# Kernel optimization log

Hardware: AMD Instinct MI355X
Metric: run time of the kernel (lower is better)

The kernel has to match this reference:

```python
import jax, jax.numpy as jnp
import numpy as np

N_EMBD = 768
N_HEAD = 12
EPS = 1e-5


def _layernorm(x, g, b):
    mu = x.mean(-1, keepdims=True)
    var = ((x - mu) ** 2).mean(-1, keepdims=True)
    return (x - mu) * jax.lax.rsqrt(var + EPS) * g + b


def setup_inputs() -> dict:
    key = jax.random.key(0)
    ks = jax.random.split(key, 8)
    C = N_EMBD
    s = lambda n: 0.02
    return {
        "x": jax.random.normal(ks[0], (8, 1024, C), jnp.float32),
        "ln1_g": jnp.ones((C,), jnp.float32),
        "ln1_b": jnp.zeros((C,), jnp.float32),
        "w_attn": jax.random.normal(ks[1], (C, 3 * C), jnp.float32) * 0.02,
        "b_attn": jnp.zeros((3 * C,), jnp.float32),
        "w_proj": jax.random.normal(ks[2], (C, C), jnp.float32) * 0.02,
        "b_proj": jnp.zeros((C,), jnp.float32),
        "ln2_g": jnp.ones((C,), jnp.float32),
        "ln2_b": jnp.zeros((C,), jnp.float32),
        "w_fc": jax.random.normal(ks[3], (C, 4 * C), jnp.float32) * 0.02,
        "b_fc": jnp.zeros((4 * C,), jnp.float32),
        "w_fc2": jax.random.normal(ks[4], (4 * C, C), jnp.float32) * 0.02,
        "b_fc2": jnp.zeros((C,), jnp.float32),
    }


def reference(x, ln1_g, ln1_b, w_attn, b_attn, w_proj, b_proj,
              ln2_g, ln2_b, w_fc, b_fc, w_fc2, b_fc2):
    B, T, C = x.shape
    H = N_HEAD
    hd = C // H

    # --- attention branch (NOTE: source has NO 1/sqrt(d) scaling) ---
    h = _layernorm(x, ln1_g, ln1_b)
    qkv = h @ w_attn + b_attn                      # [B,T,3C]
    q, k, v = jnp.split(qkv, 3, axis=-1)
    q = q.reshape(B, T, H, hd)
    k = k.reshape(B, T, H, hd)
    v = v.reshape(B, T, H, hd)
    wei = jnp.einsum('bthd,bshd->bhts', q, k)      # [B,H,T,T], unscaled
    causal = jnp.tril(jnp.ones((T, T), bool))
    wei = jnp.where(causal, wei, -jnp.inf)
    wei = jax.nn.softmax(wei, axis=-1)
    out = jnp.einsum('bhts,bshd->bthd', wei, v)    # [B,T,H,hd]
    out = out.reshape(B, T, C)
    attn_out = out @ w_proj + b_proj
    x = x + attn_out

    # --- MLP branch ---
    h = _layernorm(x, ln2_g, ln2_b)
    h = jax.nn.gelu(h @ w_fc + b_fc, approximate=True)
    x = x + (h @ w_fc2 + b_fc2)
    return x
```

## Files before the change

### kernel.cpp

```cpp
#include <hip/hip_runtime.h>
#include <math.h>

#define N_EMBD 768
#define T_SEQ  1024
#define BATCH  8
#define NHEAD  12
#define HD     64
#define EPS    1e-5f
#define M_TOK  (BATCH * T_SEQ)

typedef unsigned short u16;
typedef __attribute__((ext_vector_type(8))) short          s16x8;
typedef __attribute__((ext_vector_type(8))) unsigned short u16x8;
typedef __attribute__((ext_vector_type(4))) float          f32x4;

#define GLDS(gp, lp) \
    __builtin_amdgcn_global_load_lds( \
        (const __attribute__((address_space(1))) void*)(gp), \
        (__attribute__((address_space(3))) void*)(lp), 16, 0, 0)

__device__ __forceinline__ u16 f2bf(float f) {
    unsigned int u = __float_as_uint(f);
    u += 0x7fffu + ((u >> 16) & 1u);
    return (u16)(u >> 16);
}

__global__ __launch_bounds__(256) void wconv(const float* __restrict__ in,
                                             u16* __restrict__ out, int R, int C) {
    __shared__ float tile[64][65];
    int t = threadIdx.x;
    int r0 = blockIdx.y * 64, c0 = blockIdx.x * 64;
    int rl = t >> 4, c4 = (t & 15) * 4;
#pragma unroll
    for (int i = 0; i < 4; i++) {
        float4 v = *(const float4*)(in + (size_t)(r0 + rl + i * 16) * C + c0 + c4);
        tile[rl + i * 16][c4 + 0] = v.x;
        tile[rl + i * 16][c4 + 1] = v.y;
        tile[rl + i * 16][c4 + 2] = v.z;
        tile[rl + i * 16][c4 + 3] = v.w;
    }
    __syncthreads();
#pragma unroll
    for (int i = 0; i < 4; i++) {
        int crow = rl + i * 16;
        ushort4 s4;
        s4.x = f2bf(tile[c4 + 0][crow]);
        s4.y = f2bf(tile[c4 + 1][crow]);
        s4.z = f2bf(tile[c4 + 2][crow]);
        s4.w = f2bf(tile[c4 + 3][crow]);
        *(ushort4*)(out + (size_t)(c0 + crow) * R + r0 + c4) = s4;
    }
}

__global__ __launch_bounds__(256) void ln_bf16(const float* __restrict__ x,
                                               const float* __restrict__ g,
                                               const float* __restrict__ b,
                                               u16* __restrict__ out) {
    int row = blockIdx.x;
    int tid = threadIdx.x;
    const float* xr = x + (size_t)row * N_EMBD;
    float v0 = xr[tid], v1 = xr[tid + 256], v2 = xr[tid + 512];
    float s1 = v0 + v1 + v2;
    float s2 = v0 * v0 + v1 * v1 + v2 * v2;
    __shared__ float red1[4], red2[4];
#pragma unroll
    for (int o = 32; o > 0; o >>= 1) {
        s1 += __shfl_down(s1, o);
        s2 += __shfl_down(s2, o);
    }
    if ((tid & 63) == 0) { red1[tid >> 6] = s1; red2[tid >> 6] = s2; }
    __syncthreads();
    float mean = (red1[0] + red1[1] + red1[2] + red1[3]) * (1.0f / N_EMBD);
    float ms   = (red2[0] + red2[1] + red2[2] + red2[3]) * (1.0f / N_EMBD);
    float rs = rsqrtf(ms - mean * mean + EPS);
    u16* orow = out + (size_t)row * N_EMBD;
    orow[tid]       = f2bf((v0 - mean) * rs * g[tid]       + b[tid]);
    orow[tid + 256] = f2bf((v1 - mean) * rs * g[tid + 256] + b[tid + 256]);
    orow[tid + 512] = f2bf((v2 - mean) * rs * g[tid + 512] + b[tid + 512]);
}

template <int MODE>
__global__ __launch_bounds__(256) void gemm_bf16(const u16* __restrict__ A,
                                                 const u16* __restrict__ Bt,
                                                 const float* __restrict__ bias,
                                                 const float* __restrict__ res,
                                                 void* __restrict__ outp,
                                                 int M, int N, int K) {
    __shared__ u16 As[128][64];
    __shared__ u16 Bs[128][64];
    int tid = threadIdx.x;
    int l = tid & 63, w = tid >> 6;
    int lr = l & 15, lg = l >> 4;
    int bm = blockIdx.y * 128, bn = blockIdx.x * 128;
    int wr = (w >> 1) * 64, wc = (w & 1) * 64;
    int srow = l >> 3;
    int scol = (l & 7) * 8;
    f32x4 acc[4][4] = {};
    for (int k0 = 0; k0 < K; k0 += 64) {
        __syncthreads();
#pragma unroll
        for (int i = 0; i < 4; i++) {
            int c = i * 4 + w;
            int row = c * 8 + srow;
            GLDS(A  + (size_t)(bm + row) * K + k0 + scol, &As[c * 8][0]);
            GLDS(Bt + (size_t)(bn + row) * K + k0 + scol, &Bs[c * 8][0]);
        }
        __syncthreads();
#pragma unroll
        for (int kk = 0; kk < 2; kk++) {
            s16x8 af[4], bf[4];
#pragma unroll
            for (int i = 0; i < 4; i++) {
                af[i] = *(const s16x8*)&As[wr + i * 16 + lr][kk * 32 + lg * 8];
                bf[i] = *(const s16x8*)&Bs[wc + i * 16 + lr][kk * 32 + lg * 8];
            }
#pragma unroll
            for (int mi = 0; mi < 4; mi++)
#pragma unroll
                for (int nj = 0; nj < 4; nj++)
                    acc[mi][nj] = __builtin_amdgcn_mfma_f32_16x16x32_bf16(
                        af[mi], bf[nj], acc[mi][nj], 0, 0, 0);
        }
    }
#pragma unroll
    for (int mi = 0; mi < 4; mi++)
#pragma unroll
        for (int nj = 0; nj < 4; nj++)
#pragma unroll
            for (int r = 0; r < 4; r++) {
                int row = bm + wr + mi * 16 + lg * 4 + r;
                int col = bn + wc + nj * 16 + lr;
                float v = acc[mi][nj][r] + bias[col];
                if (MODE == 1) {
                    float u = v + 0.044715f * v * v * v;
                    v = 0.5f * v * (1.0f + tanhf(0.7978845608028654f * u));
                }
                if (MODE == 2) {
                    v += res[(size_t)row * N + col];
                    ((float*)outp)[(size_t)row * N + col] = v;
                } else {
                    ((u16*)outp)[(size_t)row * N + col] = f2bf(v);
                }
            }
}

#define QBLK 128
#define SBLK 64
__global__ __launch_bounds__(256) void attn_mfma(const u16* __restrict__ qkv,
                                                 u16* __restrict__ outp) {
    __shared__ u16 Kl[SBLK][64];
    __shared__ u16 Vt[HD][72];
    __shared__ u16 Pl[4][32][72];
    int tid = threadIdx.x;
    int w = tid >> 6, l = tid & 63;
    int lr = l & 15, lg = l >> 4;
    int h = blockIdx.y, b = blockIdx.z;
    size_t bbase = (size_t)b * T_SEQ * (3 * N_EMBD);

    for (int half = 0; half < 2; half++) {
        int qt = half == 0 ? blockIdx.x : 7 - blockIdx.x;
        int q0 = qt * QBLK;

        s16x8 qf[2][2];
#pragma unroll
        for (int rg = 0; rg < 2; rg++)
#pragma unroll
            for (int kk = 0; kk < 2; kk++) {
                int row = q0 + w * 32 + rg * 16 + lr;
                qf[rg][kk] = *(const s16x8*)(qkv + bbase + (size_t)row * (3 * N_EMBD) +
                                             h * HD + kk * 32 + lg * 8);
            }
        f32x4 oacc[2][4] = {};
        float mrun[2][4], lrun[2][4];
#pragma unroll
        for (int rg = 0; rg < 2; rg++)
#pragma unroll
            for (int r = 0; r < 4; r++) { mrun[rg][r] = -1e30f; lrun[rg][r] = 0.f; }

        int nt = 2 * qt + 2;
        for (int st = 0; st < nt; st++) {
            int s0 = st * SBLK;
#pragma unroll
            for (int i = 0; i < 2; i++) {
                int c = i * 4 + w;
                int row = c * 8 + (l >> 3);
                GLDS(qkv + bbase + (size_t)(s0 + row) * (3 * N_EMBD) + N_EMBD + h * HD + (l & 7) * 8,
                     &Kl[c * 8][0]);
            }
#pragma unroll
            for (int i = 0; i < 2; i++) {
                int c = i * 256 + tid;
                int sr = c >> 3, d0 = (c & 7) * 8;
                u16x8 vv = *(const u16x8*)(qkv + bbase + (size_t)(s0 + sr) * (3 * N_EMBD) +
                                           2 * N_EMBD + h * HD + d0);
                int sz = ((sr >> 3) ^ (d0 >> 3)) * 8 + (sr & 7);
#pragma unroll
                for (int j = 0; j < 8; j++) Vt[d0 + j][sz] = vv[j];
            }
            __syncthreads();
            f32x4 sacc[2][4] = {};
#pragma unroll
            for (int kk = 0; kk < 2; kk++) {
                s16x8 kf[4];
#pragma unroll
                for (int nj = 0; nj < 4; nj++)
                    kf[nj] = *(const s16x8*)&Kl[nj * 16 + lr][kk * 32 + lg * 8];
#pragma unroll
                for (int rg = 0; rg < 2; rg++)
#pragma unroll
                    for (int nj = 0; nj < 4; nj++)
                        sacc[rg][nj] = __builtin_amdgcn_mfma_f32_16x16x32_bf16(
                            qf[rg][kk], kf[nj], sacc[rg][nj], 0, 0, 0);
            }
#pragma unroll
            for (int rg = 0; rg < 2; rg++) {
                int qrow0 = q0 + w * 32 + rg * 16 + lg * 4;
                float mx[4];
#pragma unroll
                for (int r = 0; r < 4; r++) {
                    int qi = qrow0 + r;
                    float mv = -1e30f;
#pragma unroll
                    for (int nj = 0; nj < 4; nj++) {
                        int si = s0 + nj * 16 + lr;
                        float v = sacc[rg][nj][r];
                        v = (si <= qi) ? v : -1e30f;
                        sacc[rg][nj][r] = v;
                        mv = fmaxf(mv, v);
                    }
                    mx[r] = mv;
                }
#pragma unroll
                for (int d = 1; d < 16; d <<= 1)
#pragma unroll
                    for (int r = 0; r < 4; r++) mx[r] = fmaxf(mx[r], __shfl_xor(mx[r], d, 64));
                float rs[4];
#pragma unroll
                for (int r = 0; r < 4; r++) {
                    float mnew = fmaxf(mrun[rg][r], mx[r]);
                    float sc = __expf(mrun[rg][r] - mnew);
                    mrun[rg][r] = mnew;
                    float sum = 0.f;
#pragma unroll
                    for (int nj = 0; nj < 4; nj++) {
                        float p = __expf(sacc[rg][nj][r] - mnew);
                        sacc[rg][nj][r] = p;
                        sum += p;
                    }
                    rs[r] = sum;
                    lrun[rg][r] *= sc;
#pragma unroll
                    for (int nj = 0; nj < 4; nj++) oacc[rg][nj][r] *= sc;
                }
#pragma unroll
                for (int d = 1; d < 16; d <<= 1)
#pragma unroll
                    for (int r = 0; r < 4; r++) rs[r] += __shfl_xor(rs[r], d, 64);
#pragma unroll
                for (int r = 0; r < 4; r++) lrun[rg][r] += rs[r];
#pragma unroll
                for (int nj = 0; nj < 4; nj++)
#pragma unroll
                    for (int r = 0; r < 4; r++)
                        Pl[w][rg * 16 + lg * 4 + r][nj * 16 + lr] = f2bf(sacc[rg][nj][r]);
            }
            __syncthreads();
#pragma unroll
            for (int kk = 0; kk < 2; kk++) {
                s16x8 af[2], vf[4];
#pragma unroll
                for (int rg = 0; rg < 2; rg++)
                    af[rg] = *(const s16x8*)&Pl[w][rg * 16 + lr][kk * 32 + lg * 8];
#pragma unroll
                for (int nj = 0; nj < 4; nj++) {
                    int d = nj * 16 + lr;
                    int gs = (kk * 4 + lg) ^ (d >> 3);
                    vf[nj] = *(const s16x8*)&Vt[d][gs * 8];
                }
#pragma unroll
                for (int rg = 0; rg < 2; rg++)
#pragma unroll
                    for (int nj = 0; nj < 4; nj++)
                        oacc[rg][nj] = __builtin_amdgcn_mfma_f32_16x16x32_bf16(
                            af[rg], vf[nj], oacc[rg][nj], 0, 0, 0);
            }
            __syncthreads();
        }
#pragma unroll
        for (int rg = 0; rg < 2; rg++)
#pragma unroll
            for (int nj = 0; nj < 4; nj++)
#pragma unroll
                for (int r = 0; r < 4; r++) {
                    int row = q0 + w * 32 + rg * 16 + lg * 4 + r;
                    float v = oacc[rg][nj][r] / lrun[rg][r];
                    outp[(size_t)(b * T_SEQ + row) * N_EMBD + h * HD + nj * 16 + lr] = f2bf(v);
                }
    }
}

extern "C" void kernel_launch(void* const* d_in, const int* in_sizes, int n_in,
                              void* d_out, int out_size, void* d_ws, size_t ws_size,
                              hipStream_t stream) {
    (void)in_sizes; (void)n_in; (void)out_size; (void)ws_size;
    const float* x      = (const float*)d_in[0];
    const float* ln1_g  = (const float*)d_in[1];
    const float* ln1_b  = (const float*)d_in[2];
    const float* w_attn = (const float*)d_in[3];
    const float* b_attn = (const float*)d_in[4];
    const float* w_proj = (const float*)d_in[5];
    const float* b_proj = (const float*)d_in[6];
    const float* ln2_g  = (const float*)d_in[7];
    const float* ln2_b  = (const float*)d_in[8];
    const float* w_fc   = (const float*)d_in[9];
    const float* b_fc   = (const float*)d_in[10];
    const float* w_fc2  = (const float*)d_in[11];
    const float* b_fc2  = (const float*)d_in[12];
    float* out = (float*)d_out;
    u16* ws = (u16*)d_ws;

    u16* wTa  = ws;
    u16* wTp  = wTa + (size_t)2304 * 768;
    u16* wTf  = wTp + (size_t)768 * 768;
    u16* wTf2 = wTf + (size_t)3072 * 768;
    u16* hbuf = wTf2 + (size_t)768 * 3072;
    u16* abuf = hbuf + (size_t)M_TOK * N_EMBD;
    u16* big  = abuf + (size_t)M_TOK * N_EMBD;

    wconv<<<dim3(2304 / 64, 768 / 64), 256, 0, stream>>>(w_attn, wTa, 768, 2304);
    wconv<<<dim3(768 / 64, 768 / 64), 256, 0, stream>>>(w_proj, wTp, 768, 768);
    wconv<<<dim3(3072 / 64, 768 / 64), 256, 0, stream>>>(w_fc, wTf, 768, 3072);
    wconv<<<dim3(768 / 64, 3072 / 64), 256, 0, stream>>>(w_fc2, wTf2, 3072, 768);
    ln_bf16<<<M_TOK, 256, 0, stream>>>(x, ln1_g, ln1_b, hbuf);
    gemm_bf16<0><<<dim3(18, 64), 256, 0, stream>>>(hbuf, wTa, b_attn, nullptr, big,
                                                   M_TOK, 3 * N_EMBD, N_EMBD);
    attn_mfma<<<dim3(T_SEQ / QBLK / 2, NHEAD, BATCH), 256, 0, stream>>>(big, abuf);
    gemm_bf16<2><<<dim3(6, 64), 256, 0, stream>>>(abuf, wTp, b_proj, x, out,
                                                  M_TOK, N_EMBD, N_EMBD);
    ln_bf16<<<M_TOK, 256, 0, stream>>>(out, ln2_g, ln2_b, hbuf);
    gemm_bf16<1><<<dim3(24, 64), 256, 0, stream>>>(hbuf, wTf, b_fc, nullptr, big,
                                                   M_TOK, 4 * N_EMBD, N_EMBD);
    gemm_bf16<2><<<dim3(6, 64), 256, 0, stream>>>(big, wTf2, b_fc2, out, out,
                                                  M_TOK, N_EMBD, 4 * N_EMBD);
}
```

Before: 456.5 us.

## Double-buffer GEMM LDS tiles, swizzle block order, and use exp-based GELU

The bf16 GEMM now keeps two LDS buffers per operand. It issues the asynchronous global-to-LDS loads for the next K tile before running the MFMAs on the current one, so memory latency overlaps compute, and one barrier per iteration is removed. Workgroup IDs are remapped in groups of 8 to change which output tiles run together, aiming for better L2 reuse across the chiplets. The tanh GELU is rewritten in the equivalent form v - v/(1+exp(2a)) using __expf, which is cheaper. LDS usage doubles, which can lower occupancy.

After: 439.7 us. -3.7%, faster.

```diff
diff --git a/kernel.cpp b/kernel.cpp
--- a/kernel.cpp
+++ b/kernel.cpp
@@ -86,33 +86,46 @@
                                                  const float* __restrict__ res,
                                                  void* __restrict__ outp,
                                                  int M, int N, int K) {
-    __shared__ u16 As[128][64];
-    __shared__ u16 Bs[128][64];
+    __shared__ u16 As[2][128][64];
+    __shared__ u16 Bs[2][128][64];
     int tid = threadIdx.x;
     int l = tid & 63, w = tid >> 6;
     int lr = l & 15, lg = l >> 4;
-    int bm = blockIdx.y * 128, bn = blockIdx.x * 128;
+    int gx = gridDim.x, nwg = gx * gridDim.y;
+    int bid = blockIdx.y * gx + blockIdx.x;
+    int swz = (bid & 7) * (nwg >> 3) + (bid >> 3);
+    int bm = (swz / gx) * 128, bn = (swz % gx) * 128;
     int wr = (w >> 1) * 64, wc = (w & 1) * 64;
-    int srow = l >> 3;
-    int scol = (l & 7) * 8;
+    int srow = l >> 3, scol = (l & 7) * 8;
     f32x4 acc[4][4] = {};
-    for (int k0 = 0; k0 < K; k0 += 64) {
+    int nt = K / 64;
+#pragma unroll
+    for (int i = 0; i < 4; i++) {
+        int c = i * 4 + w;
+        int row = c * 8 + srow;
+        GLDS(A  + (size_t)(bm + row) * K + scol, &As[0][c * 8][0]);
+        GLDS(Bt + (size_t)(bn + row) * K + scol, &Bs[0][c * 8][0]);
+    }
+    int cur = 0;
+    for (int t = 0; t < nt; t++) {
         __syncthreads();
-#pragma unroll
-        for (int i = 0; i < 4; i++) {
-            int c = i * 4 + w;
-            int row = c * 8 + srow;
-            GLDS(A  + (size_t)(bm + row) * K + k0 + scol, &As[c * 8][0]);
-            GLDS(Bt + (size_t)(bn + row) * K + k0 + scol, &Bs[c * 8][0]);
+        if (t + 1 < nt) {
+            int k0 = (t + 1) * 64;
+#pragma unroll
+            for (int i = 0; i < 4; i++) {
+                int c = i * 4 + w;
+                int row = c * 8 + srow;
+                GLDS(A  + (size_t)(bm + row) * K + k0 + scol, &As[cur ^ 1][c * 8][0]);
+                GLDS(Bt + (size_t)(bn + row) * K + k0 + scol, &Bs[cur ^ 1][c * 8][0]);
+            }
         }
-        __syncthreads();
 #pragma unroll
         for (int kk = 0; kk < 2; kk++) {
             s16x8 af[4], bf[4];
 #pragma unroll
             for (int i = 0; i < 4; i++) {
-                af[i] = *(const s16x8*)&As[wr + i * 16 + lr][kk * 32 + lg * 8];
-                bf[i] = *(const s16x8*)&Bs[wc + i * 16 + lr][kk * 32 + lg * 8];
+                af[i] = *(const s16x8*)&As[cur][wr + i * 16 + lr][kk * 32 + lg * 8];
+                bf[i] = *(const s16x8*)&Bs[cur][wc + i * 16 + lr][kk * 32 + lg * 8];
             }
 #pragma unroll
             for (int mi = 0; mi < 4; mi++)
@@ -121,6 +134,7 @@
                     acc[mi][nj] = __builtin_amdgcn_mfma_f32_16x16x32_bf16(
                         af[mi], bf[nj], acc[mi][nj], 0, 0, 0);
         }
+        cur ^= 1;
     }
 #pragma unroll
     for (int mi = 0; mi < 4; mi++)
@@ -132,8 +146,8 @@
                 int col = bn + wc + nj * 16 + lr;
                 float v = acc[mi][nj][r] + bias[col];
                 if (MODE == 1) {
-                    float u = v + 0.044715f * v * v * v;
-                    v = 0.5f * v * (1.0f + tanhf(0.7978845608028654f * u));
+                    float u = 1.5957691216057308f * (v + 0.044715f * v * v * v);
+                    v = v - v / (1.0f + __expf(u));
                 }
                 if (MODE == 2) {
                     v += res[(size_t)row * N + col];
@@ -160,7 +174,6 @@
     for (int half = 0; half < 2; half++) {
         int qt = half == 0 ? blockIdx.x : 7 - blockIdx.x;
         int q0 = qt * QBLK;
-
         s16x8 qf[2][2];
 #pragma unroll
         for (int rg = 0; rg < 2; rg++)
```

## Double-buffer GEMM LDS tiles, XOR-swizzle LDS layout, cheaper GELU via exp

Applied to the files above, without the earlier changes.

The GEMM now keeps two LDS buffers and issues the global-to-LDS loads for tile t+2 while computing tile t, using vmcnt waits and raw barriers in place of the two __syncthreads per k-step. The global source column is XOR-swizzled by row so the MFMA fragment reads from LDS avoid bank conflicts, and the attention K tile gets the same swizzle. The tanh-based GELU is rewritten algebraically as v - v/(1+exp(2u)) using __expf. Together these aim to hide memory latency and cut LDS conflicts, at the cost of twice the GEMM LDS footprint (lower occupancy) and slightly different GELU rounding.

Result: faster. 395.4 us (-13.4%).

```diff
diff --git a/kernel.cpp b/kernel.cpp
--- a/kernel.cpp
+++ b/kernel.cpp
@@ -79,6 +79,18 @@
     orow[tid + 512] = f2bf((v2 - mean) * rs * g[tid + 512] + b[tid + 512]);
 }
 
+#define STAGE_G(buf, t)                                                              \
+    do {                                                                             \
+        int k0_ = (t) * 64;                                                          \
+        _Pragma("unroll")                                                            \
+        for (int i_ = 0; i_ < 4; i_++) {                                             \
+            int c_ = i_ * 4 + w;                                                     \
+            int row_ = c_ * 8 + srow;                                                \
+            GLDS(A  + (size_t)(bm + row_) * K + k0_ + scolx, &As[buf][c_ * 8][0]);   \
+            GLDS(Bt + (size_t)(bn + row_) * K + k0_ + scolx, &Bs[buf][c_ * 8][0]);   \
+        }                                                                            \
+    } while (0)
+
 template <int MODE>
 __global__ __launch_bounds__(256) void gemm_bf16(const u16* __restrict__ A,
                                                  const u16* __restrict__ Bt,
@@ -86,33 +98,33 @@
                                                  const float* __restrict__ res,
                                                  void* __restrict__ outp,
                                                  int M, int N, int K) {
-    __shared__ u16 As[128][64];
-    __shared__ u16 Bs[128][64];
+    __shared__ u16 As[2][128][64];
+    __shared__ u16 Bs[2][128][64];
     int tid = threadIdx.x;
     int l = tid & 63, w = tid >> 6;
     int lr = l & 15, lg = l >> 4;
     int bm = blockIdx.y * 128, bn = blockIdx.x * 128;
     int wr = (w >> 1) * 64, wc = (w & 1) * 64;
     int srow = l >> 3;
-    int scol = (l & 7) * 8;
+    int scolx = ((l & 7) * 8) ^ (srow * 8);
     f32x4 acc[4][4] = {};
-    for (int k0 = 0; k0 < K; k0 += 64) {
-        __syncthreads();
-#pragma unroll
-        for (int i = 0; i < 4; i++) {
-            int c = i * 4 + w;
-            int row = c * 8 + srow;
-            GLDS(A  + (size_t)(bm + row) * K + k0 + scol, &As[c * 8][0]);
-            GLDS(Bt + (size_t)(bn + row) * K + k0 + scol, &Bs[c * 8][0]);
-        }
-        __syncthreads();
+    int nt = K / 64;
+    STAGE_G(0, 0);
+    STAGE_G(1, 1);
+    for (int t = 0; t < nt; t++) {
+        if (t < nt - 1) asm volatile("s_waitcnt vmcnt(8)" ::: "memory");
+        else            asm volatile("s_waitcnt vmcnt(0)" ::: "memory");
+        __builtin_amdgcn_s_barrier();
+        __builtin_amdgcn_sched_barrier(0);
+        int cur = t & 1;
 #pragma unroll
         for (int kk = 0; kk < 2; kk++) {
             s16x8 af[4], bf[4];
+            int rc = (kk * 32 + lg * 8) ^ ((lr & 7) * 8);
 #pragma unroll
             for (int i = 0; i < 4; i++) {
-                af[i] = *(const s16x8*)&As[wr + i * 16 + lr][kk * 32 + lg * 8];
-                bf[i] = *(const s16x8*)&Bs[wc + i * 16 + lr][kk * 32 + lg * 8];
+                af[i] = *(const s16x8*)&As[cur][wr + i * 16 + lr][rc];
+                bf[i] = *(const s16x8*)&Bs[cur][wc + i * 16 + lr][rc];
             }
 #pragma unroll
             for (int mi = 0; mi < 4; mi++)
@@ -121,6 +133,8 @@
                     acc[mi][nj] = __builtin_amdgcn_mfma_f32_16x16x32_bf16(
                         af[mi], bf[nj], acc[mi][nj], 0, 0, 0);
         }
+        __builtin_amdgcn_s_barrier();
+        if (t + 2 < nt) STAGE_G(cur, t + 2);
     }
 #pragma unroll
     for (int mi = 0; mi < 4; mi++)
@@ -132,8 +146,8 @@
                 int col = bn + wc + nj * 16 + lr;
                 float v = acc[mi][nj][r] + bias[col];
                 if (MODE == 1) {
-                    float u = v + 0.044715f * v * v * v;
-                    v = 0.5f * v * (1.0f + tanhf(0.7978845608028654f * u));
+                    float u = 1.5957691216057308f * (v + 0.044715f * v * v * v);
+                    v = v - v / (1.0f + __expf(u));
                 }
                 if (MODE == 2) {
                     v += res[(size_t)row * N + col];
@@ -156,11 +170,12 @@
     int lr = l & 15, lg = l >> 4;
     int h = blockIdx.y, b = blockIdx.z;
     size_t bbase = (size_t)b * T_SEQ * (3 * N_EMBD);
+    int srow = l >> 3;
+    int scolx = ((l & 7) * 8) ^ (srow * 8);
 
     for (int half = 0; half < 2; half++) {
         int qt = half == 0 ? blockIdx.x : 7 - blockIdx.x;
         int q0 = qt * QBLK;
-
         s16x8 qf[2][2];
 #pragma unroll
         for (int rg = 0; rg < 2; rg++)
@@ -183,8 +198,8 @@
 #pragma unroll
             for (int i = 0; i < 2; i++) {
                 int c = i * 4 + w;
-                int row = c * 8 + (l >> 3);
-                GLDS(qkv + bbase + (size_t)(s0 + row) * (3 * N_EMBD) + N_EMBD + h * HD + (l & 7) * 8,
+                GLDS(qkv + bbase + (size_t)(s0 + c * 8 + srow) * (3 * N_EMBD) + N_EMBD +
+                         h * HD + scolx,
                      &Kl[c * 8][0]);
             }
 #pragma unroll
@@ -202,9 +217,10 @@
 #pragma unroll
             for (int kk = 0; kk < 2; kk++) {
                 s16x8 kf[4];
+                int rc = (kk * 32 + lg * 8) ^ ((lr & 7) * 8);
 #pragma unroll
                 for (int nj = 0; nj < 4; nj++)
-                    kf[nj] = *(const s16x8*)&Kl[nj * 16 + lr][kk * 32 + lg * 8];
+                    kf[nj] = *(const s16x8*)&Kl[nj * 16 + lr][rc];
 #pragma unroll
                 for (int rg = 0; rg < 2; rg++)
 #pragma unroll
```
